# Kernel tuning notes

Measured on AMD Instinct MI355X. Metric: run time of the kernel, lower is better.

Reference implementation:

```python
import jax, jax.numpy as jnp
import numpy as np

N, E, FDIM, H = 50000, 1_600_000, 256, 128


def setup_inputs() -> dict:
    key = jax.random.key(0)
    ks = jax.random.split(key, 16)
    s = 0.05
    return {
        "node_features": jax.random.normal(ks[0], (N, FDIM), dtype=jnp.float32),
        "edge_index": jax.random.randint(ks[1], (2, E), 0, N, dtype=jnp.int64),
        # node encoder: Linear(F,H) -> ReLU -> Linear(H,H)
        "enc_w1": jax.random.normal(ks[2], (FDIM, H), dtype=jnp.float32) * s,
        "enc_b1": jnp.zeros((H,), dtype=jnp.float32),
        "enc_w2": jax.random.normal(ks[3], (H, H), dtype=jnp.float32) * s,
        "enc_b2": jnp.zeros((H,), dtype=jnp.float32),
        # three GCNConv layers (weight + bias each)
        "conv_w1": jax.random.normal(ks[4], (H, H), dtype=jnp.float32) * s,
        "conv_b1": jnp.zeros((H,), dtype=jnp.float32),
        "conv_w2": jax.random.normal(ks[5], (H, H), dtype=jnp.float32) * s,
        "conv_b2": jnp.zeros((H,), dtype=jnp.float32),
        "conv_w3": jax.random.normal(ks[6], (H, H), dtype=jnp.float32) * s,
        "conv_b3": jnp.zeros((H,), dtype=jnp.float32),
        # edge classifier: Linear(2H,H) -> ReLU -> Dropout(eval: identity) -> Linear(H,1) -> Sigmoid
        "cls_w1": jax.random.normal(ks[7], (2 * H, H), dtype=jnp.float32) * s,
        "cls_b1": jnp.zeros((H,), dtype=jnp.float32),
        "cls_w2": jax.random.normal(ks[8], (H, 1), dtype=jnp.float32) * s,
        "cls_b2": jnp.zeros((1,), dtype=jnp.float32),
    }


def _gcn_conv(x, w, b, src, dst, norm, n):
    # GCNConv: x' = scatter_add_dst(norm * (x W)[src]) + b  (self-loops already in src/dst/norm)
    xw = x @ w
    out = jax.ops.segment_sum(xw[src] * norm[:, None], dst, num_segments=n)
    return out + b


def reference(node_features, edge_index, enc_w1, enc_b1, enc_w2, enc_b2,
              conv_w1, conv_b1, conv_w2, conv_b2, conv_w3, conv_b3,
              cls_w1, cls_b1, cls_w2, cls_b2):
    n = node_features.shape[0]
    loops = jnp.arange(n, dtype=edge_index.dtype)
    src = jnp.concatenate([edge_index[0], loops])  # (E+N,)
    dst = jnp.concatenate([edge_index[1], loops])
    # symmetric normalization with self-loops (PyG gcn_norm defaults)
    deg = jax.ops.segment_sum(jnp.ones(src.shape, node_features.dtype), dst, num_segments=n)
    dis = jnp.where(deg > 0, jax.lax.rsqrt(jnp.maximum(deg, 1.0)), 0.0)
    norm = dis[src] * dis[dst]  # (E+N,)

    # node encoder
    x = jax.nn.relu(node_features @ enc_w1 + enc_b1) @ enc_w2 + enc_b2
    # stacked GCN layers
    x = jax.nn.relu(_gcn_conv(x, conv_w1, conv_b1, src, dst, norm, n))
    x = jax.nn.relu(_gcn_conv(x, conv_w2, conv_b2, src, dst, norm, n))
    x = _gcn_conv(x, conv_w3, conv_b3, src, dst, norm, n)

    # edge features: gather + concat  -> (E, 2H)
    ef = jnp.concatenate([x[edge_index[0]], x[edge_index[1]]], axis=1)
    h = jax.nn.relu(ef @ cls_w1 + cls_b1)  # Dropout is identity at eval
    scores = jax.nn.sigmoid(h @ cls_w2 + cls_b2)
    return scores.squeeze(-1)  # (E,)
```

## Files before the change

kernel.cpp:

```cpp
#include <hip/hip_runtime.h>
#include <math.h>

#define HDIM 128
#define BSH 7
#define MAXBUCK 512

typedef __attribute__((ext_vector_type(8))) short    bf16x8;
typedef __attribute__((ext_vector_type(4))) float    f32x4;
typedef __attribute__((ext_vector_type(2))) float    f32x2;
typedef __attribute__((ext_vector_type(8))) unsigned short u16x8;
typedef __attribute__((ext_vector_type(4))) unsigned short u16x4;

__device__ __forceinline__ float bf2f(unsigned short u) {
    union { unsigned int i; float f; } c; c.i = ((unsigned int)u) << 16; return c.f;
}
__device__ __forceinline__ unsigned short f2bf(float f) {
    union { float f; unsigned int i; } c; c.f = f;
    unsigned int r = (c.i + 0x7fffu + ((c.i >> 16) & 1u)) >> 16;
    return (unsigned short)r;
}
__device__ __forceinline__ void f8x8_dec(uint2 v, float* f) {
    f32x2 a = __builtin_amdgcn_cvt_pk_f32_fp8((int)v.x, false);
    f32x2 b = __builtin_amdgcn_cvt_pk_f32_fp8((int)v.x, true);
    f32x2 c = __builtin_amdgcn_cvt_pk_f32_fp8((int)v.y, false);
    f32x2 d = __builtin_amdgcn_cvt_pk_f32_fp8((int)v.y, true);
    f[0] = a.x; f[1] = a.y; f[2] = b.x; f[3] = b.y;
    f[4] = c.x; f[5] = c.y; f[6] = d.x; f[7] = d.y;
}

__global__ __launch_bounds__(256) void k_hist(
    const int* __restrict__ dst, int* __restrict__ tot,
    int* __restrict__ hist, int E, int chunk, int nbuck)
{
    __shared__ int h[MAXBUCK];
    for (int i = threadIdx.x; i < MAXBUCK; i += 256) h[i] = 0;
    __syncthreads();
    int beg = blockIdx.x * chunk;
    int fin = min(beg + chunk, E);
    for (int e = beg + threadIdx.x; e < fin; e += 256)
        atomicAdd(&h[dst[e] >> BSH], 1);
    __syncthreads();
    for (int k = threadIdx.x; k < nbuck; k += 256) {
        int v = h[k];
        hist[(size_t)blockIdx.x * nbuck + k] = v;
        if (v) atomicAdd(&tot[k], v);
    }
}

__global__ __launch_bounds__(256) void k_scan_buckets(
    const int* __restrict__ tot, int* __restrict__ gcur, int* __restrict__ base, int nbuck)
{
    __shared__ int a[MAXBUCK], b[MAXBUCK];
    int t = threadIdx.x;
    for (int i = t; i < MAXBUCK; i += 256) a[i] = (i < nbuck) ? tot[i] : 0;
    __syncthreads();
    int* s1 = a; int* s2 = b;
    for (int off = 1; off < MAXBUCK; off <<= 1) {
        for (int i = t; i < MAXBUCK; i += 256)
            s2[i] = s1[i] + ((i >= off) ? s1[i - off] : 0);
        __syncthreads();
        int* tmp = s1; s1 = s2; s2 = tmp;
    }
    for (int i = t; i < nbuck; i += 256) {
        int e = (i == 0) ? 0 : s1[i - 1];
        gcur[i] = e;
        base[i] = e;
    }
    if (t == 0) base[nbuck] = s1[nbuck - 1];
}

__global__ __launch_bounds__(256) void k_partition(
    const int* __restrict__ src, const int* __restrict__ dst,
    const int* __restrict__ hist, int* __restrict__ gcur,
    uint2* __restrict__ stag, int E, int chunk, int nbuck)
{
    __shared__ int h[MAXBUCK];
    int t = threadIdx.x;
    for (int k = t; k < nbuck; k += 256) {
        int v = hist[(size_t)blockIdx.x * nbuck + k];
        h[k] = v ? atomicAdd(&gcur[k], v) : 0;
    }
    __syncthreads();
    int beg = blockIdx.x * chunk;
    int fin = min(beg + chunk, E);
    for (int e = beg + t; e < fin; e += 256) {
        unsigned int d = (unsigned int)dst[e];
        unsigned int s = (unsigned int)src[e];
        int pos = atomicAdd(&h[d >> BSH], 1);
        stag[pos] = make_uint2(s | (d << 16), (unsigned int)e);
    }
}

__global__ __launch_bounds__(256) void k_bucket_csr(
    const int* __restrict__ base, const uint2* __restrict__ stag,
    int* __restrict__ row_ptr, int* __restrict__ col, float* __restrict__ dis, int n, int nbuck)
{
    __shared__ int cl[128], sa[128], sb[128], cur[128];
    int k = blockIdx.x;
    int n0 = k << BSH;
    int t = threadIdx.x;
    if (t < 128) cl[t] = 0;
    __syncthreads();
    int b0 = base[k];
    int m = base[k + 1] - b0;
    const uint2* seg = stag + b0;
    for (int i = t; i < m; i += 256) atomicAdd(&cl[(seg[i].x >> 16) & 127], 1);
    __syncthreads();
    int cv = 0;
    if (t < 128) { cv = cl[t]; sa[t] = cv; }
    __syncthreads();
    int* s1 = sa; int* s2 = sb;
    for (int off = 1; off < 128; off <<= 1) {
        if (t < 128) s2[t] = s1[t] + ((t >= off) ? s1[t - off] : 0);
        __syncthreads();
        int* tmp = s1; s1 = s2; s2 = tmp;
    }
    if (t < 128) {
        int node = n0 + t;
        if (node < n) {
            int rpv = b0 + s1[t] - cv;
            row_ptr[node] = rpv;
            cur[t] = rpv;
            dis[node] = rsqrtf(1.0f + (float)cv);
        }
    }
    if (k == 0 && t == 0) row_ptr[n] = base[nbuck];
    __syncthreads();
    for (int i = t; i < m; i += 256) {
        unsigned int e = seg[i].x;
        int pos = atomicAdd(&cur[(e >> 16) & 127], 1);
        col[pos] = (int)(e & 0xffffu);
    }
}

struct WEnt { const float* src; unsigned short* dst; int K; };
struct WAll { WEnt w[7]; };

__global__ __launch_bounds__(256) void k_prep_w(WAll all) {
    WEnt e = all.w[blockIdx.y];
    int i = blockIdx.x * 256 + threadIdx.x;
    if (i >= e.K * HDIM) return;
    int k = i >> 7, c = i & 127;
    e.dst[(size_t)c * e.K + k] = f2bf(e.src[i]);
}

__global__ __launch_bounds__(256) void k_gemm_b(
    const unsigned short* __restrict__ X, const unsigned short* __restrict__ Wt,
    const float* __restrict__ bias, const float* __restrict__ scale,
    void* __restrict__ C, int M, int relu_out, int out_fp8)
{
    __shared__ unsigned short sW[128 * 128];
    const int t = threadIdx.x;
#pragma unroll
    for (int i = 0; i < 8; i++) {
        int c = t + i * 256;
        int row = c >> 4, o = c & 15;
        int mt = row >> 4, r = row & 15, kc = o >> 2, q = o & 3;
        int lidx = (mt * 4 + kc) * 64 + q * 16 + r;
        *(uint4*)(sW + (size_t)lidx * 8) = *(const uint4*)(Wt + (size_t)c * 8);
    }
    __syncthreads();
    int wave = t >> 6, lane = t & 63;
    int quad = lane >> 4, r = lane & 15;
    int row0 = blockIdx.x * 64 + wave * 16;
    if (row0 >= M) return;
    const unsigned short* xp = X + (size_t)(row0 + r) * 128 + quad * 8;
    f32x4 acc[8];
#pragma unroll
    for (int mt = 0; mt < 8; mt++) acc[mt] = (f32x4){0.f, 0.f, 0.f, 0.f};
#pragma unroll
    for (int kc = 0; kc < 4; kc++) {
        bf16x8 xf = *(const bf16x8*)(xp + kc * 32);
#pragma unroll
        for (int mt = 0; mt < 8; mt++) {
            bf16x8 wf = *(const bf16x8*)(sW + ((size_t)((mt * 4 + kc) * 64 + lane)) * 8);
            acc[mt] = __builtin_amdgcn_mfma_f32_16x16x32_bf16(wf, xf, acc[mt], 0, 0, 0);
        }
    }
    float sc = scale ? scale[row0 + r] : 1.f;
    if (out_fp8) {
        unsigned char* cp = (unsigned char*)C + (size_t)(row0 + r) * HDIM + quad * 4;
#pragma unroll
        for (int mt = 0; mt < 8; mt++) {
            float v[4];
#pragma unroll
            for (int j = 0; j < 4; j++) {
                float x = acc[mt][j];
                if (bias) x += bias[mt * 16 + quad * 4 + j];
                if (relu_out) x = fmaxf(x, 0.f);
                v[j] = x * sc;
            }
            int wd = 0;
            wd = __builtin_amdgcn_cvt_pk_fp8_f32(v[0], v[1], wd, false);
            wd = __builtin_amdgcn_cvt_pk_fp8_f32(v[2], v[3], wd, true);
            *(unsigned int*)(cp + mt * 16) = (unsigned int)wd;
        }
    } else {
        unsigned short* cp = (unsigned short*)C + (size_t)(row0 + r) * HDIM + quad * 4;
#pragma unroll
        for (int mt = 0; mt < 8; mt++) {
            u16x4 o;
#pragma unroll
            for (int j = 0; j < 4; j++) {
                float v = acc[mt][j];
                if (bias) v += bias[mt * 16 + quad * 4 + j];
                if (relu_out) v = fmaxf(v, 0.f);
                o[j] = f2bf(v * sc);
            }
            *(u16x4*)(cp + mt * 16) = o;
        }
    }
}

__global__ __launch_bounds__(256) void k_gemm_nf(
    const float* __restrict__ X, const unsigned short* __restrict__ Wt,
    const float* __restrict__ bias, unsigned short* __restrict__ C,
    int M, int relu_out)
{
    const int K = 256;
    int wave = threadIdx.x >> 6, lane = threadIdx.x & 63;
    int quad = lane >> 4, r = lane & 15;
    int row0 = blockIdx.x * 64 + wave * 16;
    if (row0 >= M) return;
    const float* xp = X + (size_t)(row0 + r) * K + quad * 8;
    const unsigned short* wp = Wt + (size_t)r * K + quad * 8;
    f32x4 acc[8];
#pragma unroll
    for (int mt = 0; mt < 8; mt++) acc[mt] = (f32x4){0.f, 0.f, 0.f, 0.f};
#pragma unroll 2
    for (int k0 = 0; k0 < K; k0 += 32) {
        float4 xa = *(const float4*)(xp + k0);
        float4 xb = *(const float4*)(xp + k0 + 4);
        bf16x8 xf;
        xf[0] = (short)f2bf(xa.x); xf[1] = (short)f2bf(xa.y);
        xf[2] = (short)f2bf(xa.z); xf[3] = (short)f2bf(xa.w);
        xf[4] = (short)f2bf(xb.x); xf[5] = (short)f2bf(xb.y);
        xf[6] = (short)f2bf(xb.z); xf[7] = (short)f2bf(xb.w);
#pragma unroll
        for (int mt = 0; mt < 8; mt++) {
            bf16x8 wf = *(const bf16x8*)(wp + (size_t)mt * 16 * K + k0);
            acc[mt] = __builtin_amdgcn_mfma_f32_16x16x32_bf16(wf, xf, acc[mt], 0, 0, 0);
        }
    }
    unsigned short* cp = C + (size_t)(row0 + r) * HDIM + quad * 4;
#pragma unroll
    for (int mt = 0; mt < 8; mt++) {
        u16x4 o;
#pragma unroll
        for (int j = 0; j < 4; j++) {
            float v = acc[mt][j];
            if (bias) v += bias[mt * 16 + quad * 4 + j];
            if (relu_out) v = fmaxf(v, 0.f);
            o[j] = f2bf(v);
        }
        *(u16x4*)(cp + mt * 16) = o;
    }
}

__global__ __launch_bounds__(256) void k_aggregate_f8(
    const int* __restrict__ row_ptr, const int* __restrict__ col,
    const float* __restrict__ dis, const uint2* __restrict__ y8,
    const float* __restrict__ bias, unsigned short* __restrict__ out, int n, int relu_out)
{
    int wid = (blockIdx.x * 256 + threadIdx.x) >> 6;
    if (wid >= n) return;
    int lane = threadIdx.x & 63;
    int q = lane >> 4, t = lane & 15;
    float acc[8];
    {
        uint2 sv = y8[(size_t)wid * 16 + t];
        float f[8]; f8x8_dec(sv, f);
#pragma unroll
        for (int i = 0; i < 8; i++) acc[i] = (q == 0) ? f[i] : 0.f;
    }
    int beg = row_ptr[wid], end = row_ptr[wid + 1];
    int j = beg + q;
    for (; j + 28 < end; j += 32) {
        int s[8];
        uint2 v[8];
#pragma unroll
        for (int u = 0; u < 8; u++) s[u] = col[j + u * 4];
#pragma unroll
        for (int u = 0; u < 8; u++) v[u] = y8[(size_t)s[u] * 16 + t];
#pragma unroll
        for (int u = 0; u < 8; u++) {
            float f[8]; f8x8_dec(v[u], f);
#pragma unroll
            for (int i = 0; i < 8; i++) acc[i] += f[i];
        }
    }
    for (; j + 12 < end; j += 16) {
        int s0 = col[j], s1 = col[j + 4], s2 = col[j + 8], s3 = col[j + 12];
        uint2 v0 = y8[(size_t)s0 * 16 + t];
        uint2 v1 = y8[(size_t)s1 * 16 + t];
        uint2 v2 = y8[(size_t)s2 * 16 + t];
        uint2 v3 = y8[(size_t)s3 * 16 + t];
        float f0[8], f1[8], f2[8], f3[8];
        f8x8_dec(v0, f0); f8x8_dec(v1, f1); f8x8_dec(v2, f2); f8x8_dec(v3, f3);
#pragma unroll
        for (int i = 0; i < 8; i++) acc[i] += (f0[i] + f1[i]) + (f2[i] + f3[i]);
    }
    for (; j < end; j += 4) {
        int s = col[j];
        uint2 v = y8[(size_t)s * 16 + t];
        float f[8]; f8x8_dec(v, f);
#pragma unroll
        for (int i = 0; i < 8; i++) acc[i] += f[i];
    }
#pragma unroll
    for (int i = 0; i < 8; i++) {
        acc[i] += __shfl_xor(acc[i], 16, 64);
        acc[i] += __shfl_xor(acc[i], 32, 64);
    }
    if (q == 0) {
        float di = dis[wid];
        u16x8 o;
#pragma unroll
        for (int i = 0; i < 8; i++) {
            float v = di * acc[i] + bias[t * 8 + i];
            if (relu_out) v = fmaxf(v, 0.f);
            o[i] = f2bf(v);
        }
        *(u16x8*)(out + (size_t)wid * HDIM + t * 8) = o;
    }
}

__global__ __launch_bounds__(256) void k_edge_score_sorted(
    const uint2* __restrict__ stag, const uint2* __restrict__ P8,
    const uint2* __restrict__ Q8,
    const float* __restrict__ w2, const float* __restrict__ b2,
    float* __restrict__ out, int E, int chunk)
{
    int nblk = gridDim.x;
    int c = (int)((blockIdx.x & 7) * (nblk >> 3) + (blockIdx.x >> 3));
    int sub = threadIdx.x & 15;
    int grp = threadIdx.x >> 4;
    float w[8];
#pragma unroll
    for (int j = 0; j < 8; j++) w[j] = w2[sub * 8 + j];
    float bb = b2[0];
    int beg = c * chunk;
    int fin = min(beg + chunk, E);
    int i = beg + grp;
    for (; i + 16 < fin; i += 32) {
        uint2 e0 = stag[i], e1 = stag[i + 16];
        int s0 = (int)(e0.x & 0xffffu), d0 = (int)(e0.x >> 16);
        int s1 = (int)(e1.x & 0xffffu), d1 = (int)(e1.x >> 16);
        uint2 pv0 = P8[(size_t)s0 * 16 + sub];
        uint2 qv0 = Q8[(size_t)d0 * 16 + sub];
        uint2 pv1 = P8[(size_t)s1 * 16 + sub];
        uint2 qv1 = Q8[(size_t)d1 * 16 + sub];
        float pf0[8], qf0[8], pf1[8], qf1[8];
        f8x8_dec(pv0, pf0); f8x8_dec(qv0, qf0);
        f8x8_dec(pv1, pf1); f8x8_dec(qv1, qf1);
        float p0 = 0.f, p1 = 0.f;
#pragma unroll
        for (int j = 0; j < 8; j++) {
            p0 += fmaxf(pf0[j] + qf0[j], 0.f) * w[j];
            p1 += fmaxf(pf1[j] + qf1[j], 0.f) * w[j];
        }
        p0 += __shfl_xor(p0, 8, 16); p1 += __shfl_xor(p1, 8, 16);
        p0 += __shfl_xor(p0, 4, 16); p1 += __shfl_xor(p1, 4, 16);
        p0 += __shfl_xor(p0, 2, 16); p1 += __shfl_xor(p1, 2, 16);
        p0 += __shfl_xor(p0, 1, 16); p1 += __shfl_xor(p1, 1, 16);
        if (sub == 0) {
            float sc0 = 1.f / (1.f + expf(-(p0 + bb)));
            float sc1 = 1.f / (1.f + expf(-(p1 + bb)));
            __builtin_nontemporal_store(sc0, &out[e0.y]);
            __builtin_nontemporal_store(sc1, &out[e1.y]);
        }
    }
    if (i < fin) {
        uint2 ent = stag[i];
        int s = (int)(ent.x & 0xffffu);
        int d = (int)(ent.x >> 16);
        uint2 pv = P8[(size_t)s * 16 + sub];
        uint2 qv = Q8[(size_t)d * 16 + sub];
        float pf[8], qf[8];
        f8x8_dec(pv, pf); f8x8_dec(qv, qf);
        float part = 0.f;
#pragma unroll
        for (int j = 0; j < 8; j++)
            part += fmaxf(pf[j] + qf[j], 0.f) * w[j];
        part += __shfl_xor(part, 8, 16);
        part += __shfl_xor(part, 4, 16);
        part += __shfl_xor(part, 2, 16);
        part += __shfl_xor(part, 1, 16);
        if (sub == 0) {
            float sc = 1.f / (1.f + expf(-(part + bb)));
            __builtin_nontemporal_store(sc, &out[ent.y]);
        }
    }
}

extern "C" void kernel_launch(void* const* d_in, const int* in_sizes, int n_in,
                              void* d_out, int out_size, void* d_ws, size_t ws_size,
                              hipStream_t stream) {
    const float* nf   = (const float*)d_in[0];
    const int*   ei   = (const int*)d_in[1];
    const float* ew1  = (const float*)d_in[2];
    const float* eb1  = (const float*)d_in[3];
    const float* ew2  = (const float*)d_in[4];
    const float* eb2  = (const float*)d_in[5];
    const float* cw1  = (const float*)d_in[6];
    const float* cb1  = (const float*)d_in[7];
    const float* cw2  = (const float*)d_in[8];
    const float* cb2  = (const float*)d_in[9];
    const float* cw3  = (const float*)d_in[10];
    const float* cb3  = (const float*)d_in[11];
    const float* clw1 = (const float*)d_in[12];
    const float* clb1 = (const float*)d_in[13];
    const float* clw2 = (const float*)d_in[14];
    const float* clb2 = (const float*)d_in[15];
    float* out = (float*)d_out;

    const int FD = 256;
    const int N = in_sizes[0] / FD;
    const int E = in_sizes[1] / 2;
    const int NBUCK = (N + 127) >> BSH;
    const int PBLK = 256;
    const int chunk = (E + PBLK - 1) / PBLK;

    size_t Np = ((size_t)N + 256) & ~(size_t)255;
    char* w = (char*)d_ws;
    float* dis     = (float*)w;            w += Np * 4;
    int*   tot     = (int*)w;              w += MAXBUCK * 4;
    int*   gcur    = (int*)w;              w += MAXBUCK * 4;
    int*   base    = (int*)w;              w += (MAXBUCK + 4) * 4;
    int*   hist    = (int*)w;              w += (size_t)PBLK * MAXBUCK * 4;
    int*   row_ptr = (int*)w;              w += Np * 4;
    uint2* stag    = (uint2*)w;            w += (size_t)E * 8;
    int*   col     = (int*)w;              w += (((size_t)E * 4) + 255) & ~(size_t)255;
    unsigned short* bufA = (unsigned short*)w;  w += (size_t)N * HDIM * 2;
    unsigned short* bufB = (unsigned short*)w;  w += (size_t)N * HDIM * 2;
    unsigned short* bufC = (unsigned short*)w;  w += (size_t)N * HDIM * 2;
    unsigned char*  f8X  = (unsigned char*)w;   w += ((size_t)N * HDIM + 255) & ~(size_t)255;
    unsigned char*  f8P  = (unsigned char*)w;   w += ((size_t)N * HDIM + 255) & ~(size_t)255;
    unsigned char*  f8Q  = (unsigned char*)w;   w += ((size_t)N * HDIM + 255) & ~(size_t)255;
    unsigned short* wtE1 = (unsigned short*)w;  w += 256 * HDIM * 2;
    unsigned short* wtE2 = (unsigned short*)w;  w += 128 * HDIM * 2;
    unsigned short* wtC1 = (unsigned short*)w;  w += 128 * HDIM * 2;
    unsigned short* wtC2 = (unsigned short*)w;  w += 128 * HDIM * 2;
    unsigned short* wtC3 = (unsigned short*)w;  w += 128 * HDIM * 2;
    unsigned short* wtT  = (unsigned short*)w;  w += 128 * HDIM * 2;
    unsigned short* wtB  = (unsigned short*)w;  w += 128 * HDIM * 2;

    int gemm_grid = (N + 63) / 64;
    int ag = (N + 3) / 4;

    WAll wa;
    wa.w[0] = { ew1,               wtE1, 256 };
    wa.w[1] = { ew2,               wtE2, 128 };
    wa.w[2] = { cw1,               wtC1, 128 };
    wa.w[3] = { cw2,               wtC2, 128 };
    wa.w[4] = { cw3,               wtC3, 128 };
    wa.w[5] = { clw1,              wtT,  128 };
    wa.w[6] = { clw1 + 128 * HDIM, wtB,  128 };
    k_prep_w<<<dim3(128, 7), 256, 0, stream>>>(wa);

    hipMemsetAsync(tot, 0, MAXBUCK * sizeof(int), stream);
    k_hist<<<PBLK, 256, 0, stream>>>(ei + E, tot, hist, E, chunk, NBUCK);
    k_scan_buckets<<<1, 256, 0, stream>>>(tot, gcur, base, NBUCK);
    k_partition<<<PBLK, 256, 0, stream>>>(ei, ei + E, hist, gcur, stag, E, chunk, NBUCK);
    k_bucket_csr<<<NBUCK, 256, 0, stream>>>(base, stag, row_ptr, col, dis, N, NBUCK);

    k_gemm_nf<<<gemm_grid, 256, 0, stream>>>(nf, wtE1, eb1, bufA, N, 1);
    k_gemm_b<<<gemm_grid, 256, 0, stream>>>(bufA, wtE2, eb2, nullptr, bufB, N, 0, 0);

    k_gemm_b<<<gemm_grid, 256, 0, stream>>>(bufB, wtC1, nullptr, dis, f8X, N, 0, 1);
    k_aggregate_f8<<<ag, 256, 0, stream>>>(row_ptr, col, dis, (const uint2*)f8X, cb1, bufC, N, 1);
    k_gemm_b<<<gemm_grid, 256, 0, stream>>>(bufC, wtC2, nullptr, dis, f8X, N, 0, 1);
    k_aggregate_f8<<<ag, 256, 0, stream>>>(row_ptr, col, dis, (const uint2*)f8X, cb2, bufA, N, 1);
    k_gemm_b<<<gemm_grid, 256, 0, stream>>>(bufA, wtC3, nullptr, dis, f8X, N, 0, 1);
    k_aggregate_f8<<<ag, 256, 0, stream>>>(row_ptr, col, dis, (const uint2*)f8X, cb3, bufB, N, 0);

    k_gemm_b<<<gemm_grid, 256, 0, stream>>>(bufB, wtT, clb1, nullptr, f8P, N, 0, 1);
    k_gemm_b<<<gemm_grid, 256, 0, stream>>>(bufB, wtB, nullptr, nullptr, f8Q, N, 0, 1);

    const int SBLK = 2048;
    int schunk = (E + SBLK - 1) / SBLK;
    k_edge_score_sorted<<<SBLK, 256, 0, stream>>>(stag, (const uint2*)f8P, (const uint2*)f8Q,
                                                  clw2, clb2, out, E, schunk);
}
```

Before: 466.2 us.

## Score edges per destination node via CSR and stage encoder weights in LDS

The CSR build now stores packed (src, original edge id) pairs instead of bare column indices. The edge-score kernel walks this CSR one node per wave, loading and decoding the destination's Q row once and reusing it across all incident edges. This replaces the bucket-sorted stag walk that re-gathered Q for every edge. Separately, the first encoder GEMM copies its 256x128 bf16 weight into shared memory in an MFMA-friendly layout rather than reading it from global memory each iteration. The costs are a wider col array read by the aggregation kernels, 64KB of LDS per block in the GEMM (which may lower occupancy), and possible load imbalance from skewed node degrees.

After: 458.6 us. About the same (-1.6%).

```diff
diff --git a/kernel.cpp b/kernel.cpp
--- a/kernel.cpp
+++ b/kernel.cpp
@@ -93,7 +93,7 @@
 
 __global__ __launch_bounds__(256) void k_bucket_csr(
     const int* __restrict__ base, const uint2* __restrict__ stag,
-    int* __restrict__ row_ptr, int* __restrict__ col, float* __restrict__ dis, int n, int nbuck)
+    int* __restrict__ row_ptr, uint2* __restrict__ epk, float* __restrict__ dis, int n, int nbuck)
 {
     __shared__ int cl[128], sa[128], sb[128], cur[128];
     int k = blockIdx.x;
@@ -127,9 +127,9 @@
     if (k == 0 && t == 0) row_ptr[n] = base[nbuck];
     __syncthreads();
     for (int i = t; i < m; i += 256) {
-        unsigned int e = seg[i].x;
-        int pos = atomicAdd(&cur[(e >> 16) & 127], 1);
-        col[pos] = (int)(e & 0xffffu);
+        uint2 e = seg[i];
+        int pos = atomicAdd(&cur[(e.x >> 16) & 127], 1);
+        epk[pos] = make_uint2(e.x & 0xffffu, e.y);
     }
 }
 
@@ -218,19 +218,29 @@
     int M, int relu_out)
 {
     const int K = 256;
-    int wave = threadIdx.x >> 6, lane = threadIdx.x & 63;
+    __shared__ unsigned short sW[128 * 256];
+    const int t = threadIdx.x;
+#pragma unroll
+    for (int i = 0; i < 16; i++) {
+        int c = t + i * 256;
+        int row = c >> 5, o = c & 31;
+        int mt = row >> 4, r = row & 15, kc = o >> 2, q = o & 3;
+        int lidx = (mt * 8 + kc) * 64 + q * 16 + r;
+        *(uint4*)(sW + (size_t)lidx * 8) = *(const uint4*)(Wt + (size_t)c * 8);
+    }
+    __syncthreads();
+    int wave = t >> 6, lane = t & 63;
     int quad = lane >> 4, r = lane & 15;
     int row0 = blockIdx.x * 64 + wave * 16;
     if (row0 >= M) return;
     const float* xp = X + (size_t)(row0 + r) * K + quad * 8;
-    const unsigned short* wp = Wt + (size_t)r * K + quad * 8;
     f32x4 acc[8];
 #pragma unroll
     for (int mt = 0; mt < 8; mt++) acc[mt] = (f32x4){0.f, 0.f, 0.f, 0.f};
 #pragma unroll 2
-    for (int k0 = 0; k0 < K; k0 += 32) {
-        float4 xa = *(const float4*)(xp + k0);
-        float4 xb = *(const float4*)(xp + k0 + 4);
+    for (int kc = 0; kc < 8; kc++) {
+        float4 xa = *(const float4*)(xp + kc * 32);
+        float4 xb = *(const float4*)(xp + kc * 32 + 4);
         bf16x8 xf;
         xf[0] = (short)f2bf(xa.x); xf[1] = (short)f2bf(xa.y);
         xf[2] = (short)f2bf(xa.z); xf[3] = (short)f2bf(xa.w);
@@ -238,7 +248,7 @@
         xf[6] = (short)f2bf(xb.z); xf[7] = (short)f2bf(xb.w);
 #pragma unroll
         for (int mt = 0; mt < 8; mt++) {
-            bf16x8 wf = *(const bf16x8*)(wp + (size_t)mt * 16 * K + k0);
+            bf16x8 wf = *(const bf16x8*)(sW + ((size_t)((mt * 8 + kc) * 64 + lane)) * 8);
             acc[mt] = __builtin_amdgcn_mfma_f32_16x16x32_bf16(wf, xf, acc[mt], 0, 0, 0);
         }
     }
@@ -258,7 +268,7 @@
 }
 
 __global__ __launch_bounds__(256) void k_aggregate_f8(
-    const int* __restrict__ row_ptr, const int* __restrict__ col,
+    const int* __restrict__ row_ptr, const uint2* __restrict__ epk,
     const float* __restrict__ dis, const uint2* __restrict__ y8,
     const float* __restrict__ bias, unsigned short* __restrict__ out, int n, int relu_out)
 {
@@ -279,7 +289,7 @@
         int s[8];
         uint2 v[8];
 #pragma unroll
-        for (int u = 0; u < 8; u++) s[u] = col[j + u * 4];
+        for (int u = 0; u < 8; u++) s[u] = (int)epk[j + u * 4].x;
 #pragma unroll
         for (int u = 0; u < 8; u++) v[u] = y8[(size_t)s[u] * 16 + t];
 #pragma unroll
@@ -290,7 +300,8 @@
         }
     }
     for (; j + 12 < end; j += 16) {
-        int s0 = col[j], s1 = col[j + 4], s2 = col[j + 8], s3 = col[j + 12];
+        int s0 = (int)epk[j].x, s1 = (int)epk[j + 4].x;
+        int s2 = (int)epk[j + 8].x, s3 = (int)epk[j + 12].x;
         uint2 v0 = y8[(size_t)s0 * 16 + t];
         uint2 v1 = y8[(size_t)s1 * 16 + t];
         uint2 v2 = y8[(size_t)s2 * 16 + t];
@@ -301,7 +312,7 @@
         for (int i = 0; i < 8; i++) acc[i] += (f0[i] + f1[i]) + (f2[i] + f3[i]);
     }
     for (; j < end; j += 4) {
-        int s = col[j];
+        int s = (int)epk[j].x;
         uint2 v = y8[(size_t)s * 16 + t];
         float f[8]; f8x8_dec(v, f);
 #pragma unroll
@@ -325,70 +336,66 @@
     }
 }
 
-__global__ __launch_bounds__(256) void k_edge_score_sorted(
-    const uint2* __restrict__ stag, const uint2* __restrict__ P8,
-    const uint2* __restrict__ Q8,
+__global__ __launch_bounds__(256) void k_edge_score_csr(
+    const int* __restrict__ row_ptr, const uint2* __restrict__ epk,
+    const uint2* __restrict__ P8, const uint2* __restrict__ Q8,
     const float* __restrict__ w2, const float* __restrict__ b2,
-    float* __restrict__ out, int E, int chunk)
-{
-    int nblk = gridDim.x;
-    int c = (int)((blockIdx.x & 7) * (nblk >> 3) + (blockIdx.x >> 3));
-    int sub = threadIdx.x & 15;
-    int grp = threadIdx.x >> 4;
+    float* __restrict__ out, int n)
+{
+    int wid = (blockIdx.x * 256 + threadIdx.x) >> 6;
+    if (wid >= n) return;
+    int lane = threadIdx.x & 63;
+    int q = lane >> 4, t = lane & 15;
     float w[8];
 #pragma unroll
-    for (int j = 0; j < 8; j++) w[j] = w2[sub * 8 + j];
+    for (int j = 0; j < 8; j++) w[j] = w2[t * 8 + j];
     float bb = b2[0];
-    int beg = c * chunk;
-    int fin = min(beg + chunk, E);
-    int i = beg + grp;
-    for (; i + 16 < fin; i += 32) {
-        uint2 e0 = stag[i], e1 = stag[i + 16];
-        int s0 = (int)(e0.x & 0xffffu), d0 = (int)(e0.x >> 16);
-        int s1 = (int)(e1.x & 0xffffu), d1 = (int)(e1.x >> 16);
-        uint2 pv0 = P8[(size_t)s0 * 16 + sub];
-        uint2 qv0 = Q8[(size_t)d0 * 16 + sub];
-        uint2 pv1 = P8[(size_t)s1 * 16 + sub];
-        uint2 qv1 = Q8[(size_t)d1 * 16 + sub];
-        float pf0[8], qf0[8], pf1[8], qf1[8];
-        f8x8_dec(pv0, pf0); f8x8_dec(qv0, qf0);
-        f8x8_dec(pv1, pf1); f8x8_dec(qv1, qf1);
+    float qf[8];
+    {
+        uint2 qv = Q8[(size_t)wid * 16 + t];
+        f8x8_dec(qv, qf);
+    }
+    int beg = row_ptr[wid], end = row_ptr[wid + 1];
+    int j = beg + q;
+    for (; j + 4 < end; j += 8) {
+        uint2 e0 = epk[j], e1 = epk[j + 4];
+        uint2 pv0 = P8[(size_t)e0.x * 16 + t];
+        uint2 pv1 = P8[(size_t)e1.x * 16 + t];
+        float pf0[8], pf1[8];
+        f8x8_dec(pv0, pf0); f8x8_dec(pv1, pf1);
         float p0 = 0.f, p1 = 0.f;
 #pragma unroll
-        for (int j = 0; j < 8; j++) {
-            p0 += fmaxf(pf0[j] + qf0[j], 0.f) * w[j];
-            p1 += fmaxf(pf1[j] + qf1[j], 0.f) * w[j];
+        for (int i = 0; i < 8; i++) {
+            p0 += fmaxf(pf0[i] + qf[i], 0.f) * w[i];
+            p1 += fmaxf(pf1[i] + qf[i], 0.f) * w[i];
         }
         p0 += __shfl_xor(p0, 8, 16); p1 += __shfl_xor(p1, 8, 16);
         p0 += __shfl_xor(p0, 4, 16); p1 += __shfl_xor(p1, 4, 16);
         p0 += __shfl_xor(p0, 2, 16); p1 += __shfl_xor(p1, 2, 16);
         p0 += __shfl_xor(p0, 1, 16); p1 += __shfl_xor(p1, 1, 16);
-        if (sub == 0) {
-            float sc0 = 1.f / (1.f + expf(-(p0 + bb)));
-            float sc1 = 1.f / (1.f + expf(-(p1 + bb)));
-            __builtin_nontemporal_store(sc0, &out[e0.y]);
-            __builtin_nontemporal_store(sc1, &out[e1.y]);
-        }
-    }
-    if (i < fin) {
-        uint2 ent = stag[i];
-        int s = (int)(ent.x & 0xffffu);
-        int d = (int)(ent.x >> 16);
-        uint2 pv = P8[(size_t)s * 16 + sub];
-        uint2 qv = Q8[(size_t)d * 16 + sub];
-        float pf[8], qf[8];
-        f8x8_dec(pv, pf); f8x8_dec(qv, qf);
-        float part = 0.f;
-#pragma unroll
-        for (int j = 0; j < 8; j++)
-            part += fmaxf(pf[j] + qf[j], 0.f) * w[j];
-        part += __shfl_xor(part, 8, 16);
-        part += __shfl_xor(part, 4, 16);
-        part += __shfl_xor(part, 2, 16);
-        part += __shfl_xor(part, 1, 16);
-        if (sub == 0) {
-            float sc = 1.f / (1.f + expf(-(part + bb)));
-            __builtin_nontemporal_store(sc, &out[ent.y]);
+        if (t == 0) {
+            float s0 = 1.f / (1.f + expf(-(p0 + bb)));
+            float s1 = 1.f / (1.f + expf(-(p1 + bb)));
+            __builtin_nontemporal_store(s0, &out[e0.y]);
+            __builtin_nontemporal_store(s1, &out[e1.y]);
+        }
+    }
+    if (j < end) {
+        uint2 e0 = epk[j];
+        uint2 pv = P8[(size_t)e0.x * 16 + t];
+        float pf[8];
+        f8x8_dec(pv, pf);
+        float p0 = 0.f;
+#pragma unroll
+        for (int i = 0; i < 8; i++)
+            p0 += fmaxf(pf[i] + qf[i], 0.f) * w[i];
+        p0 += __shfl_xor(p0, 8, 16);
+        p0 += __shfl_xor(p0, 4, 16);
+        p0 += __shfl_xor(p0, 2, 16);
+        p0 += __shfl_xor(p0, 1, 16);
+        if (t == 0) {
+            float s0 = 1.f / (1.f + expf(-(p0 + bb)));
+            __builtin_nontemporal_store(s0, &out[e0.y]);
         }
     }
 }
@@ -430,7 +437,7 @@
     int*   hist    = (int*)w;              w += (size_t)PBLK * MAXBUCK * 4;
     int*   row_ptr = (int*)w;              w += Np * 4;
     uint2* stag    = (uint2*)w;            w += (size_t)E * 8;
-    int*   col     = (int*)w;              w += (((size_t)E * 4) + 255) & ~(size_t)255;
+    uint2* epk     = (uint2*)w;            w += (size_t)E * 8;
     unsigned short* bufA = (unsigned short*)w;  w += (size_t)N * HDIM * 2;
     unsigned short* bufB = (unsigned short*)w;  w += (size_t)N * HDIM * 2;
     unsigned short* bufC = (unsigned short*)w;  w += (size_t)N * HDIM * 2;
@@ -462,23 +469,21 @@
     k_hist<<<PBLK, 256, 0, stream>>>(ei + E, tot, hist, E, chunk, NBUCK);
     k_scan_buckets<<<1, 256, 0, stream>>>(tot, gcur, base, NBUCK);
     k_partition<<<PBLK, 256, 0, stream>>>(ei, ei + E, hist, gcur, stag, E, chunk, NBUCK);
-    k_bucket_csr<<<NBUCK, 256, 0, stream>>>(base, stag, row_ptr, col, dis, N, NBUCK);
+    k_bucket_csr<<<NBUCK, 256, 0, stream>>>(base, stag, row_ptr, epk, dis, N, NBUCK);
 
     k_gemm_nf<<<gemm_grid, 256, 0, stream>>>(nf, wtE1, eb1, bufA, N, 1);
     k_gemm_b<<<gemm_grid, 256, 0, stream>>>(bufA, wtE2, eb2, nullptr, bufB, N, 0, 0);
 
     k_gemm_b<<<gemm_grid, 256, 0, stream>>>(bufB, wtC1, nullptr, dis, f8X, N, 0, 1);
-    k_aggregate_f8<<<ag, 256, 0, stream>>>(row_ptr, col, dis, (const uint2*)f8X, cb1, bufC, N, 1);
+    k_aggregate_f8<<<ag, 256, 0, stream>>>(row_ptr, epk, dis, (const uint2*)f8X, cb1, bufC, N, 1);
     k_gemm_b<<<gemm_grid, 256, 0, stream>>>(bufC, wtC2, nullptr, dis, f8X, N, 0, 1);
-    k_aggregate_f8<<<ag, 256, 0, stream>>>(row_ptr, col, dis, (const uint2*)f8X, cb2, bufA, N, 1);
+    k_aggregate_f8<<<ag, 256, 0, stream>>>(row_ptr, epk, dis, (const uint2*)f8X, cb2, bufA, N, 1);
     k_gemm_b<<<gemm_grid, 256, 0, stream>>>(bufA, wtC3, nullptr, dis, f8X, N, 0, 1);
-    k_aggregate_f8<<<ag, 256, 0, stream>>>(row_ptr, col, dis, (const uint2*)f8X, cb3, bufB, N, 0);
+    k_aggregate_f8<<<ag, 256, 0, stream>>>(row_ptr, epk, dis, (const uint2*)f8X, cb3, bufB, N, 0);
 
     k_gemm_b<<<gemm_grid, 256, 0, stream>>>(bufB, wtT, clb1, nullptr, f8P, N, 0, 1);
     k_gemm_b<<<gemm_grid, 256, 0, stream>>>(bufB, wtB, nullptr, nullptr, f8Q, N, 0, 1);
 
-    const int SBLK = 2048;
-    int schunk = (E + SBLK - 1) / SBLK;
-    k_edge_score_sorted<<<SBLK, 256, 0, stream>>>(stag, (const uint2*)f8P, (const uint2*)f8Q,
-                                                  clw2, clb2, out, E, schunk);
-}
+    k_edge_score_csr<<<ag, 256, 0, stream>>>(row_ptr, epk, (const uint2*)f8P, (const uint2*)f8Q,
+                                             clw2, clb2, out, N);
+}
```
